# Optimization experiments

Hardware: AMD Instinct MI355X
Metric: run time of the kernel (lower is better)

## Reference

```python
import jax, jax.numpy as jnp
import numpy as np

N_NODES = 100000   # number of graph nodes
N_EDGES = 1000000  # number of edges
D_IN = 64          # input feature dim
D_OUT = 64         # output feature dim
N_RELS = 16        # number of relation types


def setup_inputs() -> dict:
    key = jax.random.key(0)
    k1, k2, k3, k4, k5 = jax.random.split(key, 5)
    feat = jax.random.normal(k1, (N_NODES, D_IN), dtype=jnp.float32)
    weight = jax.random.normal(k2, (N_RELS, D_IN, D_OUT), dtype=jnp.float32) * 0.05
    src = jax.random.randint(k3, (N_EDGES,), 0, N_NODES)
    dst = jax.random.randint(k4, (N_EDGES,), 0, N_NODES)
    etypes = jax.random.randint(k5, (N_EDGES,), 0, N_RELS)
    return {"feat": feat, "weight": weight, "src": src, "dst": dst, "etypes": etypes}


def reference(feat, weight, src, dst, etypes):
    # gather source-node features per edge: h = edges.src['h']
    h = feat[src]                                # [E, d_in]
    n_rels = weight.shape[0]
    e, d_out = h.shape[0], weight.shape[2]

    # gather_mm(h, weight, idx_b=etypes): m_e = h_e @ weight[etypes_e]
    # grouped-GEMM realized as R masked dense GEMMs (R is small, fixed);
    # avoids materializing the [E, d_in, d_out] gathered weight tensor.
    def step(m, rw):
        r, w_r = rw
        mask = jnp.where(etypes == r, 1.0, 0.0).astype(h.dtype)  # [E]
        m = m + mask[:, None] * (h @ w_r)                        # [E, d_out]
        return m, None

    m0 = jnp.zeros((e, d_out), dtype=h.dtype)
    m, _ = jax.lax.scan(step, m0, (jnp.arange(n_rels), weight))

    # update_all(..., fn.sum('m', 'h')): scatter-sum messages to dst nodes
    out = jax.ops.segment_sum(m, dst, num_segments=feat.shape[0])  # [N, d_out]
    return out
```

## Files before the change

kernel.cpp:

```cpp
#include <hip/hip_runtime.h>
#include <hip/hip_bf16.h>
#include <stdint.h>

#define NNODES 100000
#define NEDGES 1000000
#define DIM 64
#define NRELS 16
#define EPB 2048
#define NB ((NEDGES + EPB - 1) / EPB)
#define PADCAP (NEDGES + NRELS * 64)
#define MAXTILES (PADCAP / 64)
#define NDN NNODES
#define DCH 1024
#define NCHUNK ((NDN + DCH - 1) / DCH)

#define FEAT_BLKS 6250
#define W_BLKS 256
#define SETUP_BLKS (FEAT_BLKS + W_BLKS + NB)

#define WS_NEED 151805824ull

using short8  = __attribute__((ext_vector_type(8))) short;
using floatx4 = __attribute__((ext_vector_type(4))) float;
using uintx4  = __attribute__((ext_vector_type(4))) unsigned int;

__device__ __forceinline__ unsigned short f2bf(float f) {
    union { float f; uint32_t u; } v; v.f = f;
    uint32_t u = v.u;
    return (unsigned short)((u + 0x7FFFu + ((u >> 16) & 1u)) >> 16);
}
__device__ __forceinline__ float bf2f(uint32_t u16) {
    union { uint32_t u; float f; } v; v.u = u16 << 16;
    return v.f;
}
__device__ __forceinline__ uint32_t pk2(float a, float b) {
    __hip_bfloat162 h = __float22bfloat162_rn(make_float2(a, b));
    union { __hip_bfloat162 h; uint32_t u; } v; v.h = h;
    return v.u;
}

__global__ void k_setup(const float* __restrict__ feat, const float* __restrict__ W,
                        const int* __restrict__ et, const int* __restrict__ dst,
                        unsigned short* __restrict__ featB, unsigned short* __restrict__ Wt,
                        int* __restrict__ hist, int* __restrict__ dhist,
                        unsigned short* __restrict__ rank) {
    __shared__ int cnt[16];
    const int b = blockIdx.x;
    if (b < FEAT_BLKS) {
        int i = (b * 256 + threadIdx.x) * 4;
        const float4 f = *(const float4*)(feat + i);
        ushort4 o;
        o.x = f2bf(f.x); o.y = f2bf(f.y); o.z = f2bf(f.z); o.w = f2bf(f.w);
        *(ushort4*)(featB + i) = o;
    } else if (b < FEAT_BLKS + W_BLKS) {
        int t = (b - FEAT_BLKS) * 256 + threadIdx.x;
        int r = t >> 12, n = (t >> 6) & 63, k = t & 63;
        Wt[t] = f2bf(W[(r << 12) + (k << 6) + n]);
    } else {
        const int bb = b - (FEAT_BLKS + W_BLKS);
        if (threadIdx.x < 16) cnt[threadIdx.x] = 0;
        __syncthreads();
        int start = bb * EPB;
        int end = min(NEDGES, start + EPB);
        for (int i = start + threadIdx.x; i < end; i += 256) {
            atomicAdd(&cnt[et[i]], 1);
            rank[i] = (unsigned short)atomicAdd(&dhist[dst[i]], 1);
        }
        __syncthreads();
        if (threadIdx.x < 16) hist[bb * 16 + threadIdx.x] = cnt[threadIdx.x];
    }
}

__global__ void k_scan(const int* __restrict__ hist, int* __restrict__ bbase,
                       int* __restrict__ Pve) {
    __shared__ int s_cnt[16];
    __shared__ int s_P[17];
    int w = threadIdx.x >> 6;
    int lane = threadIdx.x & 63;
    int carry = 0;
    for (int c = 0; c < NB; c += 64) {
        int idx = c + lane;
        int v = (idx < NB) ? hist[idx * 16 + w] : 0;
        int x = v;
        #pragma unroll
        for (int off = 1; off < 64; off <<= 1) {
            int y = __shfl_up(x, off);
            if (lane >= off) x += y;
        }
        if (idx < NB) bbase[idx * 16 + w] = carry + x - v;
        carry += __shfl(x, 63);
    }
    if (lane == 0) s_cnt[w] = carry;
    __syncthreads();
    if (threadIdx.x == 0) {
        int p = 0;
        for (int r = 0; r < 16; ++r) {
            s_P[r] = p;
            Pve[r] = p;
            Pve[17 + r] = p + s_cnt[r];
            p += (s_cnt[r] + 63) & ~63;
        }
        s_P[16] = p;
        Pve[16] = p;
    }
    __syncthreads();
    int pw = s_P[w];
    for (int idx = lane; idx < NB; idx += 64)
        bbase[idx * 16 + w] += pw;
}

__global__ void k_dscanA(const int* __restrict__ dhist, int* __restrict__ dbase,
                         int* __restrict__ csum) {
    __shared__ int wsum[16];
    __shared__ int woff[16];
    int t = threadIdx.x;
    int i = blockIdx.x * DCH + t;
    int v = (i < NDN) ? dhist[i] : 0;
    int lane = t & 63, wv = t >> 6;
    int x = v;
    #pragma unroll
    for (int off = 1; off < 64; off <<= 1) {
        int y = __shfl_up(x, off);
        if (lane >= off) x += y;
    }
    if (lane == 63) wsum[wv] = x;
    __syncthreads();
    if (wv == 0) {
        int s = (lane < 16) ? wsum[lane] : 0;
        #pragma unroll
        for (int off = 1; off < 16; off <<= 1) {
            int y = __shfl_up(s, off);
            if (lane >= off) s += y;
        }
        if (lane < 16) woff[lane] = s - wsum[lane];
        if (lane == 15) csum[blockIdx.x] = s;
    }
    __syncthreads();
    if (i < NDN) dbase[i] = woff[wv] + x - v;
}

__global__ void k_dscanB(int* __restrict__ dbase, const int* __restrict__ csum) {
    __shared__ int soff;
    int b = blockIdx.x, t = threadIdx.x;
    if (t < 64) {
        int s = ((t < b) ? csum[t] : 0) + ((t + 64 < b) ? csum[t + 64] : 0);
        #pragma unroll
        for (int off = 32; off >= 1; off >>= 1) s += __shfl_down(s, off);
        if (t == 0) soff = s;
    }
    __syncthreads();
    int i = b * DCH + t;
    if (i < NDN) dbase[i] += soff;
}

__global__ void k_scatter(const int* __restrict__ et, const int* __restrict__ src,
                          const int* __restrict__ dst, const int* __restrict__ bbase,
                          const int* __restrict__ dbase,
                          const unsigned short* __restrict__ rank,
                          int2* __restrict__ pairS, int buildPos) {
    __shared__ int base[16];
    if (threadIdx.x < 16) base[threadIdx.x] = bbase[blockIdx.x * 16 + threadIdx.x];
    __syncthreads();
    int start = blockIdx.x * EPB;
    int end = min(NEDGES, start + EPB);
    for (int i = start + threadIdx.x; i < end; i += 256) {
        int r = et[i];
        int pos = atomicAdd(&base[r], 1);
        int d = dst[i];
        int second = buildPos ? (dbase[d] + (int)rank[i]) : d;
        pairS[pos] = make_int2(src[i], second);
    }
}

__global__ void __launch_bounds__(256)
k_computeA(const unsigned short* __restrict__ featB,
           const unsigned short* __restrict__ Wt,
           const int2* __restrict__ pairS, const int* __restrict__ Pve,
           unsigned short* __restrict__ msgE) {
    __shared__ float lds[4][16 * 68];
    const int w = threadIdx.x >> 6;
    const int t = blockIdx.x * 4 + w;
    const int base = t * 64;
    const int total = Pve[16];
    if (base >= total) return;
    int r = 0;
    while (base >= Pve[r + 1]) ++r;
    const int validEnd = Pve[17 + r];
    const int lane = threadIdx.x & 63;
    const int quad = lane >> 4;
    const int l16 = lane & 15;

    const unsigned short* wr = Wt + (r << 12);
    short8 bfr[4][2];
    #pragma unroll
    for (int tn = 0; tn < 4; ++tn)
        #pragma unroll
        for (int ks = 0; ks < 2; ++ks)
            bfr[tn][ks] = *(const short8*)(wr + ((tn * 16 + l16) << 6) + ks * 32 + quad * 8);

    const int rr = lane >> 2, seg = lane & 3;
    #pragma unroll
    for (int tm = 0; tm < 4; ++tm) {
        int row = base + tm * 16 + l16;
        int s = (row < validEnd) ? pairS[row].x : 0;
        const unsigned short* fp = featB + (s << 6) + quad * 8;
        short8 a0 = *(const short8*)(fp);
        short8 a1 = *(const short8*)(fp + 32);
        #pragma unroll
        for (int tn = 0; tn < 4; ++tn) {
            floatx4 c = {0.f, 0.f, 0.f, 0.f};
            c = __builtin_amdgcn_mfma_f32_16x16x32_bf16(a0, bfr[tn][0], c, 0, 0, 0);
            c = __builtin_amdgcn_mfma_f32_16x16x32_bf16(a1, bfr[tn][1], c, 0, 0, 0);
            #pragma unroll
            for (int j = 0; j < 4; ++j)
                lds[w][(quad * 4 + j) * 68 + tn * 16 + l16] = c[j];
        }
        int rowi = base + tm * 16 + rr;
        int p = (rowi < validEnd) ? pairS[rowi].y : -1;
        if (p >= 0) {
            const float* lp = &lds[w][rr * 68 + seg * 16];
            uintx4 o0, o1;
            o0.x = pk2(lp[0],  lp[1]);  o0.y = pk2(lp[2],  lp[3]);
            o0.z = pk2(lp[4],  lp[5]);  o0.w = pk2(lp[6],  lp[7]);
            o1.x = pk2(lp[8],  lp[9]);  o1.y = pk2(lp[10], lp[11]);
            o1.z = pk2(lp[12], lp[13]); o1.w = pk2(lp[14], lp[15]);
            uintx4* op = (uintx4*)(msgE + (size_t)p * 64 + seg * 16);
            __builtin_nontemporal_store(o0, op);
            __builtin_nontemporal_store(o1, op + 1);
        }
    }
}

__global__ void __launch_bounds__(256)
k_reduce(const unsigned short* __restrict__ msgE,
         const int* __restrict__ dbase, float* __restrict__ out) {
    int n = blockIdx.x * 4 + (threadIdx.x >> 6);
    if (n >= NDN) return;
    int lane = threadIdx.x & 63;
    int start = dbase[n];
    int end = (n + 1 < NDN) ? dbase[n + 1] : NEDGES;
    int c8 = (lane & 7) * 8;
    float a0 = 0.f, a1 = 0.f, a2 = 0.f, a3 = 0.f;
    float a4 = 0.f, a5 = 0.f, a6 = 0.f, a7 = 0.f;
    for (int row = start + (lane >> 3); row < end; row += 8) {
        const uintx4* p = (const uintx4*)(msgE + (size_t)row * 64 + c8);
        uintx4 v = __builtin_nontemporal_load(p);
        a0 += bf2f(v.x & 0xffffu); a1 += bf2f(v.x >> 16);
        a2 += bf2f(v.y & 0xffffu); a3 += bf2f(v.y >> 16);
        a4 += bf2f(v.z & 0xffffu); a5 += bf2f(v.z >> 16);
        a6 += bf2f(v.w & 0xffffu); a7 += bf2f(v.w >> 16);
    }
    #pragma unroll
    for (int m = 8; m <= 32; m <<= 1) {
        a0 += __shfl_xor(a0, m); a1 += __shfl_xor(a1, m);
        a2 += __shfl_xor(a2, m); a3 += __shfl_xor(a3, m);
        a4 += __shfl_xor(a4, m); a5 += __shfl_xor(a5, m);
        a6 += __shfl_xor(a6, m); a7 += __shfl_xor(a7, m);
    }
    if (lane < 8) {
        float* op = out + (size_t)n * 64 + lane * 8;
        *(float4*)(op)     = make_float4(a0, a1, a2, a3);
        *(float4*)(op + 4) = make_float4(a4, a5, a6, a7);
    }
}

__global__ void __launch_bounds__(256)
k_compute(const unsigned short* __restrict__ featB,
          const unsigned short* __restrict__ Wt,
          const int2* __restrict__ pairS, const int* __restrict__ Pve,
          float* __restrict__ out) {
    const int t = blockIdx.x * 4 + (threadIdx.x >> 6);
    const int base = t * 64;
    const int total = Pve[16];
    if (base >= total) return;
    int r = 0;
    while (base >= Pve[r + 1]) ++r;
    const int validEnd = Pve[17 + r];
    const int lane = threadIdx.x & 63;
    const int quad = lane >> 4;
    const int l16 = lane & 15;

    const unsigned short* wr = Wt + (r << 12);
    short8 bfr[4][2];
    #pragma unroll
    for (int tn = 0; tn < 4; ++tn)
        #pragma unroll
        for (int ks = 0; ks < 2; ++ks)
            bfr[tn][ks] = *(const short8*)(wr + ((tn * 16 + l16) << 6) + ks * 32 + quad * 8);

    #pragma unroll
    for (int tm = 0; tm < 4; ++tm) {
        int row = base + tm * 16 + l16;
        int s = (row < validEnd) ? pairS[row].x : 0;
        const unsigned short* fp = featB + (s << 6) + quad * 8;
        short8 a0 = *(const short8*)(fp);
        short8 a1 = *(const short8*)(fp + 32);
        floatx4 cc[4];
        #pragma unroll
        for (int tn = 0; tn < 4; ++tn) {
            floatx4 c = {0.f, 0.f, 0.f, 0.f};
            c = __builtin_amdgcn_mfma_f32_16x16x32_bf16(a0, bfr[tn][0], c, 0, 0, 0);
            c = __builtin_amdgcn_mfma_f32_16x16x32_bf16(a1, bfr[tn][1], c, 0, 0, 0);
            cc[tn] = c;
        }
        int pos0 = base + tm * 16 + quad * 4;
        #pragma unroll
        for (int j = 0; j < 4; ++j) {
            if (pos0 + j < validEnd) {
                int dn = pairS[pos0 + j].y;
                float* op = out + (dn << 6) + l16;
                #pragma unroll
                for (int tn = 0; tn < 4; ++tn)
                    atomicAdd(op + tn * 16, cc[tn][j]);
            }
        }
    }
}

extern "C" void kernel_launch(void* const* d_in, const int* in_sizes, int n_in,
                              void* d_out, int out_size, void* d_ws, size_t ws_size,
                              hipStream_t stream) {
    const float* feat = (const float*)d_in[0];
    const float* W    = (const float*)d_in[1];
    const int* src    = (const int*)d_in[2];
    const int* dst    = (const int*)d_in[3];
    const int* et     = (const int*)d_in[4];
    float* out = (float*)d_out;
    char* ws = (char*)d_ws;

    unsigned short* featB = (unsigned short*)(ws);
    unsigned short* Wt    = (unsigned short*)(ws + 12800000);
    int* hist  = (int*)(ws + 12931072);
    int* bbase = (int*)(ws + 12963840);
    int* Pve   = (int*)(ws + 12996608);
    int* dhist = (int*)(ws + 12996864);
    int* dbase = (int*)(ws + 13396992);
    int* csum  = (int*)(ws + 13797120);
    unsigned short* rank = (unsigned short*)(ws + 13797632);
    int2* pairS = (int2*)(ws + 15797632);
    unsigned short* msgE = (unsigned short*)(ws + 23805824);

    const int usePhases = (ws_size >= WS_NEED) ? 1 : 0;

    hipMemsetAsync(dhist, 0, NDN * sizeof(int), stream);
    k_setup<<<SETUP_BLKS, 256, 0, stream>>>(feat, W, et, dst, featB, Wt, hist, dhist, rank);
    k_scan<<<1, 1024, 0, stream>>>(hist, bbase, Pve);

    if (usePhases) {
        k_dscanA<<<NCHUNK, DCH, 0, stream>>>(dhist, dbase, csum);
        k_dscanB<<<NCHUNK, DCH, 0, stream>>>(dbase, csum);
        k_scatter<<<NB, 256, 0, stream>>>(et, src, dst, bbase, dbase, rank, pairS, 1);
        k_computeA<<<(MAXTILES + 3) / 4, 256, 0, stream>>>(featB, Wt, pairS, Pve, msgE);
        k_reduce<<<(NDN + 3) / 4, 256, 0, stream>>>(msgE, dbase, out);
    } else {
        hipMemsetAsync(d_out, 0, (size_t)out_size * sizeof(float), stream);
        k_scatter<<<NB, 256, 0, stream>>>(et, src, dst, bbase, dbase, rank, pairS, 0);
        k_compute<<<(MAXTILES + 3) / 4, 256, 0, stream>>>(featB, Wt, pairS, Pve, out);
    }
}
```

Baseline: 256.8 us.

## Replace per-node counting sort with 256-node bucket sort and LDS-atomic reduce

Instead of a global per-destination-node histogram with per-edge ranks and a full node-level prefix scan, edges are bucketed into coarse 256-node buckets using block-local LDS histograms, and each edge stores only its local node index. The reduce kernel then gives each bucket a 512-thread block that accumulates messages into a 64KB LDS tile with shared-memory float atomics, using a rotated column layout to spread bank conflicts. This removes the global atomics on dhist and the memset, but adds LDS atomic contention in reduce, large shared memory per block that limits occupancy, and a serial single-thread bucket scan.

New measurement: 635.7 us. 148% more time.

```diff
diff --git a/kernel.cpp b/kernel.cpp
--- a/kernel.cpp
+++ b/kernel.cpp
@@ -11,14 +11,14 @@
 #define PADCAP (NEDGES + NRELS * 64)
 #define MAXTILES (PADCAP / 64)
 #define NDN NNODES
-#define DCH 1024
-#define NCHUNK ((NDN + DCH - 1) / DCH)
+#define BKT 256
+#define NBKT ((NDN + BKT - 1) / BKT)
 
 #define FEAT_BLKS 6250
 #define W_BLKS 256
 #define SETUP_BLKS (FEAT_BLKS + W_BLKS + NB)
 
-#define WS_NEED 151805824ull
+#define WS_NEED 152542656ull
 
 using short8  = __attribute__((ext_vector_type(8))) short;
 using floatx4 = __attribute__((ext_vector_type(4))) float;
@@ -42,9 +42,9 @@
 __global__ void k_setup(const float* __restrict__ feat, const float* __restrict__ W,
                         const int* __restrict__ et, const int* __restrict__ dst,
                         unsigned short* __restrict__ featB, unsigned short* __restrict__ Wt,
-                        int* __restrict__ hist, int* __restrict__ dhist,
-                        unsigned short* __restrict__ rank) {
-    __shared__ int cnt[16];
+                        int* __restrict__ hist16, int* __restrict__ hist391) {
+    __shared__ int cnt16[16];
+    __shared__ int cnt391[NBKT];
     const int b = blockIdx.x;
     if (b < FEAT_BLKS) {
         int i = (b * 256 + threadIdx.x) * 4;
@@ -58,16 +58,19 @@
         Wt[t] = f2bf(W[(r << 12) + (k << 6) + n]);
     } else {
         const int bb = b - (FEAT_BLKS + W_BLKS);
-        if (threadIdx.x < 16) cnt[threadIdx.x] = 0;
+        if (threadIdx.x < 16) cnt16[threadIdx.x] = 0;
+        for (int t = threadIdx.x; t < NBKT; t += 256) cnt391[t] = 0;
         __syncthreads();
         int start = bb * EPB;
         int end = min(NEDGES, start + EPB);
         for (int i = start + threadIdx.x; i < end; i += 256) {
-            atomicAdd(&cnt[et[i]], 1);
-            rank[i] = (unsigned short)atomicAdd(&dhist[dst[i]], 1);
+            atomicAdd(&cnt16[et[i]], 1);
+            atomicAdd(&cnt391[dst[i] >> 8], 1);
         }
         __syncthreads();
-        if (threadIdx.x < 16) hist[bb * 16 + threadIdx.x] = cnt[threadIdx.x];
+        if (threadIdx.x < 16) hist16[bb * 16 + threadIdx.x] = cnt16[threadIdx.x];
+        for (int t = threadIdx.x; t < NBKT; t += 256)
+            hist391[bb * NBKT + t] = cnt391[t];
     }
 }
 
@@ -109,73 +112,71 @@
         bbase[idx * 16 + w] += pw;
 }
 
-__global__ void k_dscanA(const int* __restrict__ dhist, int* __restrict__ dbase,
-                         int* __restrict__ csum) {
-    __shared__ int wsum[16];
-    __shared__ int woff[16];
-    int t = threadIdx.x;
-    int i = blockIdx.x * DCH + t;
-    int v = (i < NDN) ? dhist[i] : 0;
-    int lane = t & 63, wv = t >> 6;
-    int x = v;
-    #pragma unroll
-    for (int off = 1; off < 64; off <<= 1) {
-        int y = __shfl_up(x, off);
-        if (lane >= off) x += y;
-    }
-    if (lane == 63) wsum[wv] = x;
-    __syncthreads();
-    if (wv == 0) {
-        int s = (lane < 16) ? wsum[lane] : 0;
-        #pragma unroll
-        for (int off = 1; off < 16; off <<= 1) {
-            int y = __shfl_up(s, off);
-            if (lane >= off) s += y;
-        }
-        if (lane < 16) woff[lane] = s - wsum[lane];
-        if (lane == 15) csum[blockIdx.x] = s;
-    }
-    __syncthreads();
-    if (i < NDN) dbase[i] = woff[wv] + x - v;
-}
-
-__global__ void k_dscanB(int* __restrict__ dbase, const int* __restrict__ csum) {
-    __shared__ int soff;
-    int b = blockIdx.x, t = threadIdx.x;
-    if (t < 64) {
-        int s = ((t < b) ? csum[t] : 0) + ((t + 64 < b) ? csum[t + 64] : 0);
-        #pragma unroll
-        for (int off = 32; off >= 1; off >>= 1) s += __shfl_down(s, off);
-        if (t == 0) soff = s;
-    }
-    __syncthreads();
-    int i = b * DCH + t;
-    if (i < NDN) dbase[i] += soff;
+__global__ void k_bscanA(const int* __restrict__ hist391, int* __restrict__ bbase391,
+                         int* __restrict__ bstart) {
+    int b = blockIdx.x * 4 + (threadIdx.x >> 6);
+    int lane = threadIdx.x & 63;
+    if (b >= NBKT) return;
+    int carry = 0;
+    for (int c = 0; c < NB; c += 64) {
+        int idx = c + lane;
+        int v = (idx < NB) ? hist391[idx * NBKT + b] : 0;
+        int x = v;
+        #pragma unroll
+        for (int off = 1; off < 64; off <<= 1) {
+            int y = __shfl_up(x, off);
+            if (lane >= off) x += y;
+        }
+        if (idx < NB) bbase391[idx * NBKT + b] = carry + x - v;
+        carry += __shfl(x, 63);
+    }
+    if (lane == 0) bstart[b] = carry;
+}
+
+__global__ void k_bscanB(int* __restrict__ bstart) {
+    if (threadIdx.x == 0) {
+        int run = 0;
+        for (int b = 0; b < NBKT; ++b) {
+            int t = bstart[b];
+            bstart[b] = run;
+            run += t;
+        }
+        bstart[NBKT] = run;
+    }
 }
 
 __global__ void k_scatter(const int* __restrict__ et, const int* __restrict__ src,
-                          const int* __restrict__ dst, const int* __restrict__ bbase,
-                          const int* __restrict__ dbase,
-                          const unsigned short* __restrict__ rank,
-                          int2* __restrict__ pairS, int buildPos) {
-    __shared__ int base[16];
-    if (threadIdx.x < 16) base[threadIdx.x] = bbase[blockIdx.x * 16 + threadIdx.x];
+                          const int* __restrict__ dst, const int* __restrict__ bbase16,
+                          const int* __restrict__ bbase391, const int* __restrict__ bstart,
+                          int2* __restrict__ pairE, unsigned short* __restrict__ dloc,
+                          int buildPos) {
+    __shared__ int base16[16];
+    __shared__ int base391[NBKT];
+    if (threadIdx.x < 16) base16[threadIdx.x] = bbase16[blockIdx.x * 16 + threadIdx.x];
+    if (buildPos)
+        for (int t = threadIdx.x; t < NBKT; t += 256)
+            base391[t] = bbase391[blockIdx.x * NBKT + t] + bstart[t];
     __syncthreads();
     int start = blockIdx.x * EPB;
     int end = min(NEDGES, start + EPB);
     for (int i = start + threadIdx.x; i < end; i += 256) {
         int r = et[i];
-        int pos = atomicAdd(&base[r], 1);
+        int pos = atomicAdd(&base16[r], 1);
         int d = dst[i];
-        int second = buildPos ? (dbase[d] + (int)rank[i]) : d;
-        pairS[pos] = make_int2(src[i], second);
+        if (buildPos) {
+            int bp = atomicAdd(&base391[d >> 8], 1);
+            pairE[pos] = make_int2(src[i], bp);
+            dloc[bp] = (unsigned short)(d & 255);
+        } else {
+            pairE[pos] = make_int2(src[i], d);
+        }
     }
 }
 
 __global__ void __launch_bounds__(256)
 k_computeA(const unsigned short* __restrict__ featB,
            const unsigned short* __restrict__ Wt,
-           const int2* __restrict__ pairS, const int* __restrict__ Pve,
+           const int2* __restrict__ pairE, const int* __restrict__ Pve,
            unsigned short* __restrict__ msgE) {
     __shared__ float lds[4][16 * 68];
     const int w = threadIdx.x >> 6;
@@ -202,7 +203,7 @@
     #pragma unroll
     for (int tm = 0; tm < 4; ++tm) {
         int row = base + tm * 16 + l16;
-        int s = (row < validEnd) ? pairS[row].x : 0;
+        int s = (row < validEnd) ? pairE[row].x : 0;
         const unsigned short* fp = featB + (s << 6) + quad * 8;
         short8 a0 = *(const short8*)(fp);
         short8 a1 = *(const short8*)(fp + 32);
@@ -216,7 +217,7 @@
                 lds[w][(quad * 4 + j) * 68 + tn * 16 + l16] = c[j];
         }
         int rowi = base + tm * 16 + rr;
-        int p = (rowi < validEnd) ? pairS[rowi].y : -1;
+        int p = (rowi < validEnd) ? pairE[rowi].y : -1;
         if (p >= 0) {
             const float* lp = &lds[w][rr * 68 + seg * 16];
             uintx4 o0, o1;
@@ -231,43 +232,49 @@
     }
 }
 
-__global__ void __launch_bounds__(256)
+__global__ void __launch_bounds__(512)
 k_reduce(const unsigned short* __restrict__ msgE,
-         const int* __restrict__ dbase, float* __restrict__ out) {
-    int n = blockIdx.x * 4 + (threadIdx.x >> 6);
-    if (n >= NDN) return;
-    int lane = threadIdx.x & 63;
-    int start = dbase[n];
-    int end = (n + 1 < NDN) ? dbase[n + 1] : NEDGES;
-    int c8 = (lane & 7) * 8;
-    float a0 = 0.f, a1 = 0.f, a2 = 0.f, a3 = 0.f;
-    float a4 = 0.f, a5 = 0.f, a6 = 0.f, a7 = 0.f;
-    for (int row = start + (lane >> 3); row < end; row += 8) {
-        const uintx4* p = (const uintx4*)(msgE + (size_t)row * 64 + c8);
-        uintx4 v = __builtin_nontemporal_load(p);
-        a0 += bf2f(v.x & 0xffffu); a1 += bf2f(v.x >> 16);
-        a2 += bf2f(v.y & 0xffffu); a3 += bf2f(v.y >> 16);
-        a4 += bf2f(v.z & 0xffffu); a5 += bf2f(v.z >> 16);
-        a6 += bf2f(v.w & 0xffffu); a7 += bf2f(v.w >> 16);
-    }
-    #pragma unroll
-    for (int m = 8; m <= 32; m <<= 1) {
-        a0 += __shfl_xor(a0, m); a1 += __shfl_xor(a1, m);
-        a2 += __shfl_xor(a2, m); a3 += __shfl_xor(a3, m);
-        a4 += __shfl_xor(a4, m); a5 += __shfl_xor(a5, m);
-        a6 += __shfl_xor(a6, m); a7 += __shfl_xor(a7, m);
-    }
-    if (lane < 8) {
-        float* op = out + (size_t)n * 64 + lane * 8;
-        *(float4*)(op)     = make_float4(a0, a1, a2, a3);
-        *(float4*)(op + 4) = make_float4(a4, a5, a6, a7);
+         const unsigned short* __restrict__ dloc,
+         const int* __restrict__ bstart, float* __restrict__ out) {
+    __shared__ float acc[BKT * 64];
+    const int b = blockIdx.x;
+    for (int i = threadIdx.x; i < BKT * 64; i += 512) acc[i] = 0.f;
+    __syncthreads();
+    const int start = bstart[b], end = bstart[b + 1];
+    const int wid = threadIdx.x >> 6;
+    const int lane = threadIdx.x & 63;
+    const int half = lane >> 5, l32 = lane & 31;
+    const uint32_t* m32 = (const uint32_t*)msgE;
+    for (int m = wid * 2 + half; start + m < end; m += 16) {
+        int row = start + m;
+        uint32_t v = __builtin_nontemporal_load(m32 + (size_t)row * 32 + l32);
+        int node = dloc[row];
+        int c0 = 2 * l32;
+        atomicAdd(&acc[node * 64 + ((c0 + node) & 63)], bf2f(v & 0xffffu));
+        atomicAdd(&acc[node * 64 + ((c0 + 1 + node) & 63)], bf2f(v >> 16));
+    }
+    __syncthreads();
+    #pragma unroll
+    for (int k = 0; k < 8; ++k) {
+        int idx = k * 512 + threadIdx.x;
+        int node = idx >> 4;
+        int c4 = (idx & 15) * 4;
+        int g = b * BKT + node;
+        if (g < NDN) {
+            float4 o;
+            o.x = acc[node * 64 + ((c4 + node) & 63)];
+            o.y = acc[node * 64 + ((c4 + 1 + node) & 63)];
+            o.z = acc[node * 64 + ((c4 + 2 + node) & 63)];
+            o.w = acc[node * 64 + ((c4 + 3 + node) & 63)];
+            *(float4*)(out + (size_t)g * 64 + c4) = o;
+        }
     }
 }
 
 __global__ void __launch_bounds__(256)
 k_compute(const unsigned short* __restrict__ featB,
           const unsigned short* __restrict__ Wt,
-          const int2* __restrict__ pairS, const int* __restrict__ Pve,
+          const int2* __restrict__ pairE, const int* __restrict__ Pve,
           float* __restrict__ out) {
     const int t = blockIdx.x * 4 + (threadIdx.x >> 6);
     const int base = t * 64;
@@ -291,7 +298,7 @@
     #pragma unroll
     for (int tm = 0; tm < 4; ++tm) {
         int row = base + tm * 16 + l16;
-        int s = (row < validEnd) ? pairS[row].x : 0;
+        int s = (row < validEnd) ? pairE[row].x : 0;
         const unsigned short* fp = featB + (s << 6) + quad * 8;
         short8 a0 = *(const short8*)(fp);
         short8 a1 = *(const short8*)(fp + 32);
@@ -307,7 +314,7 @@
         #pragma unroll
         for (int j = 0; j < 4; ++j) {
             if (pos0 + j < validEnd) {
-                int dn = pairS[pos0 + j].y;
+                int dn = pairE[pos0 + j].y;
                 float* op = out + (dn << 6) + l16;
                 #pragma unroll
                 for (int tn = 0; tn < 4; ++tn)
@@ -330,31 +337,32 @@
 
     unsigned short* featB = (unsigned short*)(ws);
     unsigned short* Wt    = (unsigned short*)(ws + 12800000);
-    int* hist  = (int*)(ws + 12931072);
-    int* bbase = (int*)(ws + 12963840);
-    int* Pve   = (int*)(ws + 12996608);
-    int* dhist = (int*)(ws + 12996864);
-    int* dbase = (int*)(ws + 13396992);
-    int* csum  = (int*)(ws + 13797120);
-    unsigned short* rank = (unsigned short*)(ws + 13797632);
-    int2* pairS = (int2*)(ws + 15797632);
-    unsigned short* msgE = (unsigned short*)(ws + 23805824);
+    int* hist16   = (int*)(ws + 12931072);
+    int* bbase16  = (int*)(ws + 12963840);
+    int* Pve      = (int*)(ws + 12996608);
+    int* hist391  = (int*)(ws + 12996864);
+    int* bbase391 = (int*)(ws + 13764864);
+    int* bstart   = (int*)(ws + 14532864);
+    unsigned short* dloc = (unsigned short*)(ws + 14534464);
+    int2* pairE   = (int2*)(ws + 16534464);
+    unsigned short* msgE = (unsigned short*)(ws + 24542656);
 
     const int usePhases = (ws_size >= WS_NEED) ? 1 : 0;
 
-    hipMemsetAsync(dhist, 0, NDN * sizeof(int), stream);
-    k_setup<<<SETUP_BLKS, 256, 0, stream>>>(feat, W, et, dst, featB, Wt, hist, dhist, rank);
-    k_scan<<<1, 1024, 0, stream>>>(hist, bbase, Pve);
+    k_setup<<<SETUP_BLKS, 256, 0, stream>>>(feat, W, et, dst, featB, Wt, hist16, hist391);
+    k_scan<<<1, 1024, 0, stream>>>(hist16, bbase16, Pve);
 
     if (usePhases) {
-        k_dscanA<<<NCHUNK, DCH, 0, stream>>>(dhist, dbase, csum);
-        k_dscanB<<<NCHUNK, DCH, 0, stream>>>(dbase, csum);
-        k_scatter<<<NB, 256, 0, stream>>>(et, src, dst, bbase, dbase, rank, pairS, 1);
-        k_computeA<<<(MAXTILES + 3) / 4, 256, 0, stream>>>(featB, Wt, pairS, Pve, msgE);
-        k_reduce<<<(NDN + 3) / 4, 256, 0, stream>>>(msgE, dbase, out);
+        k_bscanA<<<(NBKT + 3) / 4, 256, 0, stream>>>(hist391, bbase391, bstart);
+        k_bscanB<<<1, 64, 0, stream>>>(bstart);
+        k_scatter<<<NB, 256, 0, stream>>>(et, src, dst, bbase16, bbase391, bstart,
+                                          pairE, dloc, 1);
+        k_computeA<<<(MAXTILES + 3) / 4, 256, 0, stream>>>(featB, Wt, pairE, Pve, msgE);
+        k_reduce<<<NBKT, 512, 0, stream>>>(msgE, dloc, bstart, out);
     } else {
         hipMemsetAsync(d_out, 0, (size_t)out_size * sizeof(float), stream);
-        k_scatter<<<NB, 256, 0, stream>>>(et, src, dst, bbase, dbase, rank, pairS, 0);
-        k_compute<<<(MAXTILES + 3) / 4, 256, 0, stream>>>(featB, Wt, pairS, Pve, out);
-    }
-}
+        k_scatter<<<NB, 256, 0, stream>>>(et, src, dst, bbase16, bbase391, bstart,
+                                          pairE, dloc, 0);
+        k_compute<<<(MAXTILES + 3) / 4, 256, 0, stream>>>(featB, Wt, pairE, Pve, out);
+    }
+}
```
